# Performance work log

Hardware: AMD Instinct MI355X
Metric: run time of the kernel (lower is better)

Reference implementation:

```python
import jax, jax.numpy as jnp
import numpy as np

# Constants from init_kwargs
DT = 0.01
NIV = 8          # energy_input_dim[1]
HID = 64         # hidden_dims[0]
FEAT = 501       # per-field microstructure feature length (501+501=1002)


def _lin(k, fin, fout):
    return jax.random.normal(k, (fin, fout), dtype=jnp.float32) / np.sqrt(fin)


def setup_inputs() -> dict:
    key = jax.random.key(0)
    ks = jax.random.split(key, 12)
    B, T = 8192, 512
    e = jax.random.normal(ks[0], (B, T, 1), dtype=jnp.float32) * 0.1
    e_dot = jax.random.normal(ks[1], (B, T, 1), dtype=jnp.float32) * 0.1
    # positive microstructure fields (code computes nu**-1 and E/nu**2)
    E = jax.random.uniform(ks[2], (B, FEAT), minval=0.5, maxval=2.0, dtype=jnp.float32)
    nu = jax.random.uniform(ks[3], (B, FEAT), minval=0.5, maxval=2.0, dtype=jnp.float32)
    return {
        "e": e, "e_dot": e_dot, "E": E, "nu": nu,
        # EnergyFunction.B : Linear(1002,64) -> ReLU -> Linear(64,niv)
        "Bw1": _lin(ks[4], 2 * FEAT, HID), "Bb1": jnp.zeros((HID,), jnp.float32),
        "Bw2": _lin(ks[5], HID, NIV), "Bb2": jnp.zeros((NIV,), jnp.float32),
        # InverseDissipationPotential.beta : Linear(1002,64)->Softplus->Linear(64,niv)->Softplus
        "bw1": _lin(ks[6], 2 * FEAT, HID), "bb1": jnp.zeros((HID,), jnp.float32),
        "bw2": _lin(ks[7], HID, NIV), "bb2": jnp.zeros((NIV,), jnp.float32),
    }


def reference(e, e_dot, E, nu, Bw1, Bb1, Bw2, Bb2, bw1, bb1, bw2, bb2):
    # --- microstructure encoder (TrueFeatures) ---
    nu_p = 1.0 / jnp.mean(1.0 / nu, axis=1, keepdims=True)                 # [B,1]
    E_p = jnp.mean(E / nu ** 2, axis=1, keepdims=True) * nu_p ** 2         # [B,1]
    m = jnp.concatenate([E, nu], axis=-1)                                  # [B,1002]

    # Time-invariant MLP coefficients (hoisted out of the time loop)
    Bm = jax.nn.relu(m @ Bw1 + Bb1) @ Bw2 + Bb2                            # [B,NIV]
    beta = jax.nn.softplus(jax.nn.softplus(m @ bw1 + bb1) @ bw2 + bb2)     # [B,NIV]
    Bsum = jnp.sum(Bm, axis=-1, keepdims=True)                             # [B,1]

    B_, niv = Bm.shape
    xi0 = jnp.zeros((B_, niv), dtype=e.dtype)

    def step(xi, inp):
        u, p = inp                                                          # [B,1],[B,1]
        # Analytic gradients of L = sum_{b,k} Bm_bk * (0.5*E' u^2 + 0.5*(u-xi_k)^2 + 0.5*sum_j xi_j^2)
        du = u - xi                                                         # [B,NIV]
        grad_u = Bsum * E_p * u + jnp.sum(Bm * du, axis=-1, keepdims=True)  # [B,1] (s_eq)
        grad_v = -Bm * du + Bsum * xi                                       # [B,NIV] (d)
        q = -grad_v
        # Analytic gradients of potential = -0.5*nu' p^2 + 0.5*sum(beta*q^2)
        grad_p = -nu_p * p                                                  # [B,1] (s_neq)
        grad_q = beta * q                                                   # [B,NIV] (kinetics)
        stress = grad_u - grad_p
        return xi + DT * grad_q, (stress, xi)

    xs = (jnp.swapaxes(e, 0, 1), jnp.swapaxes(e_dot, 0, 1))                 # [T,B,1]
    _, (stress_t, xi_t) = jax.lax.scan(step, xi0, xs)
    stress = jnp.swapaxes(stress_t, 0, 1)                                   # [B,T,1]
    xi = jnp.swapaxes(xi_t, 0, 1)                                           # [B,T,NIV]
    return stress, xi
```

## Files before the change

### kernel.cpp

```cpp
#include <hip/hip_runtime.h>
#include <hip/hip_bf16.h>

#define FEATN 501
#define KPAD 1024
#define MSTRIDE 1032
#define NB 8192
#define NT 512
#define DTC 0.01f

typedef __attribute__((ext_vector_type(8))) short short8;
typedef __attribute__((ext_vector_type(4))) float f32x4;

__device__ __forceinline__ float softplus_f(float x) {
    return fmaxf(x, 0.f) + log1pf(expf(-fabsf(x)));
}
__device__ __forceinline__ ushort f2bf(float x) {
    __hip_bfloat16 h = __float2bfloat16(x);
    return *reinterpret_cast<ushort*>(&h);
}
__device__ __forceinline__ void gl_lds16(const void* g, void* l) {
    __builtin_amdgcn_global_load_lds(
        (const __attribute__((address_space(1))) void*)g,
        (__attribute__((address_space(3))) void*)l, 16, 0, 0);
}
__device__ __forceinline__ float dpp_add(float x, const int ctrl) {
    int s = __builtin_bit_cast(int, x);
    int y;
    switch (ctrl) {
    case 0xB1:  y = __builtin_amdgcn_update_dpp(0, s, 0xB1, 0xf, 0xf, true); break;
    case 0x4E:  y = __builtin_amdgcn_update_dpp(0, s, 0x4E, 0xf, 0xf, true); break;
    default:    y = __builtin_amdgcn_update_dpp(0, s, 0x141, 0xf, 0xf, true); break;
    }
    return x + __builtin_bit_cast(float, y);
}

__global__ __launch_bounds__(256) void wtrans_kernel(
    const float* __restrict__ Bw1, const float* __restrict__ bw1,
    ushort* __restrict__ Wt) {
    const int h = blockIdx.x;
    const float* W = (h < 64) ? Bw1 : bw1;
    const int col = h & 63;
    #pragma unroll
    for (int it = 0; it < 4; ++it) {
        const int k = it * 256 + threadIdx.x;
        const int ksrc = (k < FEATN) ? k
                       : (k >= 512 && k < 512 + FEATN) ? k - 11 : -1;
        const float v = (ksrc >= 0) ? W[(size_t)ksrc * 64 + col] : 0.f;
        Wt[(size_t)(((k >> 5) * 128 + h) * 4 + ((k >> 3) & 3)) * 8 + (k & 7)] =
            f2bf(v);
    }
}

__global__ __launch_bounds__(1024, 8) void enc_kernel(
    const float* __restrict__ E, const float* __restrict__ nu,
    const ushort* __restrict__ Wt,
    const float* __restrict__ Bb1, const float* __restrict__ bb1,
    const float* __restrict__ Bw2, const float* __restrict__ Bb2,
    const float* __restrict__ bw2, const float* __restrict__ bb2,
    float* __restrict__ cw) {
    __shared__ ushort Ml[16 * MSTRIDE];
    __shared__ float red[3][2048];
    __shared__ float hid[128][17];
    __shared__ float nups[16], Eps[16];

    const int tid = threadIdx.x;
    const int w = tid >> 6, lane = tid & 63;
    const int bb0 = blockIdx.x * 16;

    {
        const size_t base = (size_t)(bb0 + w) * FEATN;
        float s1 = 0.f, s2 = 0.f;
        for (int i = lane; i < FEATN; i += 64) {
            const float Ev = E[base + i];
            const float nv = nu[base + i];
            const float inv = 1.0f / nv;
            s1 += inv;
            s2 = fmaf(Ev, inv * inv, s2);
            Ml[w * MSTRIDE + i] = f2bf(Ev);
            Ml[w * MSTRIDE + 512 + i] = f2bf(nv);
        }
        if (lane < 11) {
            Ml[w * MSTRIDE + FEATN + lane] = 0;
            Ml[w * MSTRIDE + 512 + FEATN + lane] = 0;
        }
        #pragma unroll
        for (int o = 32; o; o >>= 1) {
            s1 += __shfl_xor(s1, o);
            s2 += __shfl_xor(s2, o);
        }
        if (lane == 0) {
            const float np = (float)FEATN / s1;
            nups[w] = np;
            Eps[w] = (s2 / (float)FEATN) * np * np;
        }
    }
    __syncthreads();

    const int g = w & 3, q = w >> 2;
    const int r15 = lane & 15, kg = lane >> 4;
    {
        const ushort* wbase = Wt + (size_t)(q * 8) * 4096;
        const int aoff = (g * 32 + r15) * 32 + kg * 8;
        const int boff = r15 * MSTRIDE + q * 256 + kg * 8;
        const int rot = blockIdx.x & 7;

        f32x4 acc0 = {0.f, 0.f, 0.f, 0.f}, acc1 = acc0;
        #pragma unroll
        for (int s = 0; s < 8; ++s) {
            const int ss = (s + rot) & 7;
            const short8 a0 = *(const short8*)(wbase + ss * 4096 + aoff);
            const short8 a1 = *(const short8*)(wbase + ss * 4096 + aoff + 512);
            const short8 b = *(const short8*)&Ml[boff + ss * 32];
            acc0 = __builtin_amdgcn_mfma_f32_16x16x32_bf16(a0, b, acc0, 0, 0, 0);
            acc1 = __builtin_amdgcn_mfma_f32_16x16x32_bf16(a1, b, acc1, 0, 0, 0);
        }
        if (q > 0) {
            *(f32x4*)&red[q - 1][(g * 64 + lane) * 8] = acc0;
            *(f32x4*)&red[q - 1][(g * 64 + lane) * 8 + 4] = acc1;
        }
        __syncthreads();
        if (q == 0) {
            #pragma unroll
            for (int p = 0; p < 3; ++p) {
                acc0 += *(const f32x4*)&red[p][(g * 64 + lane) * 8];
                acc1 += *(const f32x4*)&red[p][(g * 64 + lane) * 8 + 4];
            }
            #pragma unroll
            for (int t = 0; t < 2; ++t) {
                #pragma unroll
                for (int r = 0; r < 4; ++r) {
                    const int h = g * 32 + t * 16 + kg * 4 + r;
                    const float bias = (h < 64) ? Bb1[h] : bb1[h - 64];
                    float v = (t ? acc1[r] : acc0[r]) + bias;
                    v = (h < 64) ? fmaxf(v, 0.f) : softplus_f(v);
                    hid[h][r15] = v;
                }
            }
        }
    }
    __syncthreads();

    if (tid < 128) {
        const int bl = tid >> 3, k = tid & 7;
        float dB = 0.f, db = 0.f;
        #pragma unroll 8
        for (int h = 0; h < 64; ++h) {
            dB = fmaf(hid[h][bl], Bw2[h * 8 + k], dB);
            db = fmaf(hid[64 + h][bl], bw2[h * 8 + k], db);
        }
        const float Bm = dB + Bb2[k];
        const float be = softplus_f(db + bb2[k]);
        float Bs = Bm;
        Bs += __shfl_xor(Bs, 1);
        Bs += __shfl_xor(Bs, 2);
        Bs += __shfl_xor(Bs, 4);
        float* cb = cw + (size_t)(bb0 + bl) * 32;
        cb[k] = 1.f - DTC * be * (Bm + Bs);
        cb[8 + k] = DTC * be * Bm;
        cb[16 + k] = Bm;
        if (k == 0) {
            cb[24] = Bs * (Eps[bl] + 1.f);
            cb[25] = nups[bl];
        }
    }
}

__global__ __launch_bounds__(256) void time_kernel(
    const float* __restrict__ e, const float* __restrict__ ed,
    const float* __restrict__ cw, float* __restrict__ stress,
    float* __restrict__ xi_out) {
    __shared__ float els[4][512];
    __shared__ float pls[4][512];
    const int wv = threadIdx.x >> 6;
    const int wid = (blockIdx.x << 2) + wv;
    const int lane = threadIdx.x & 63;
    const int j = lane >> 3, k = lane & 7;

    const float* eb = e + (size_t)wid * NT;
    const float* edb = ed + (size_t)wid * NT;
    gl_lds16(eb + lane * 4, &els[wv][0]);
    gl_lds16(eb + 256 + lane * 4, &els[wv][256]);
    gl_lds16(edb + lane * 4, &pls[wv][0]);
    gl_lds16(edb + 256 + lane * 4, &pls[wv][256]);

    const float* cb = cw + (size_t)wid * 32;
    const float a = cb[k];
    const float c = cb[8 + k];
    const float Bm = cb[16 + k];
    const float sE2 = cb[24];
    const float nup = cb[25];
    asm volatile("s_waitcnt vmcnt(0)" ::: "memory");

    const float a2 = a * a, a4 = a2 * a2;
    float A = 1.f;
    if (j & 1) A *= a;
    if (j & 2) A *= a2;
    if (j & 4) A *= a4;
    float pw[8];
    {
        float run = c;
        #pragma unroll
        for (int i = 7; i >= 0; --i) {
            const bool on = (i < j);
            pw[i] = on ? run : 0.f;
            run = on ? run * a : run;
        }
    }

    float* xb = xi_out + (size_t)wid * (NT * 8);
    float* sb = stress + (size_t)wid * NT;
    const float* el = &els[wv][0];
    const float* pl = &pls[wv][0];

    float xs = 0.f;
    #pragma unroll
    for (int it = 0; it < 64; ++it) {
        const int t0 = it * 8;
        const float4 q0 = *(const float4*)(el + t0);
        const float4 q1 = *(const float4*)(el + t0 + 4);
        const float cuj = el[t0 + j];
        const float cpj = pl[t0 + j];
        float xi_j = A * xs;
        xi_j = fmaf(pw[0], q0.x, xi_j);
        xi_j = fmaf(pw[1], q0.y, xi_j);
        xi_j = fmaf(pw[2], q0.z, xi_j);
        xi_j = fmaf(pw[3], q0.w, xi_j);
        xi_j = fmaf(pw[4], q1.x, xi_j);
        xi_j = fmaf(pw[5], q1.y, xi_j);
        xi_j = fmaf(pw[6], q1.z, xi_j);
        xi_j = fmaf(pw[7], q1.w, xi_j);
        xb[t0 * 8 + lane] = xi_j;
        float r = Bm * xi_j;
        r = dpp_add(r, 0xB1);
        r = dpp_add(r, 0x4E);
        r = dpp_add(r, 0x141);
        if (k == 0)
            sb[t0 + j] = fmaf(cuj, sE2, fmaf(nup, cpj, -r));
        xs = fmaf(a, __shfl(xi_j, 56 + k), c * q1.w);
    }
}

extern "C" void kernel_launch(void* const* d_in, const int* in_sizes, int n_in,
                              void* d_out, int out_size, void* d_ws, size_t ws_size,
                              hipStream_t stream) {
    const float* e   = (const float*)d_in[0];
    const float* ed  = (const float*)d_in[1];
    const float* E   = (const float*)d_in[2];
    const float* nu  = (const float*)d_in[3];
    const float* Bw1 = (const float*)d_in[4];
    const float* Bb1 = (const float*)d_in[5];
    const float* Bw2 = (const float*)d_in[6];
    const float* Bb2 = (const float*)d_in[7];
    const float* bw1 = (const float*)d_in[8];
    const float* bb1 = (const float*)d_in[9];
    const float* bw2 = (const float*)d_in[10];
    const float* bb2 = (const float*)d_in[11];

    float* out = (float*)d_out;
    float* stress = out;
    float* xi = out + (size_t)NB * NT;
    ushort* Wt = (ushort*)d_ws;
    float* cw = (float*)((char*)d_ws + (1 << 20));

    wtrans_kernel<<<128, 256, 0, stream>>>(Bw1, bw1, Wt);
    enc_kernel<<<512, 1024, 0, stream>>>(E, nu, Wt, Bb1, bb1,
                                         Bw2, Bb2, bw2, bb2, cw);
    time_kernel<<<2048, 256, 0, stream>>>(e, ed, cw, stress, xi);
}
```

Measured before the change: 59.43 us.

## Split encoder prep into separate kernel staging bf16 features in output scratch

Moves the per-row reductions and the bf16 conversion of E/nu out of the encoder into a separate 2048-block prep kernel. That kernel writes the packed features into the unused xi output buffer and the nu_p/E_p scalars into the coefficient workspace. The encoder then loads its tile with direct global-to-LDS copies and a lower occupancy hint. The aim is to spread the memory-bound prep over more blocks, at the cost of an extra launch and a global round trip. It relies on time_kernel later overwriting xi.

```diff
diff --git a/kernel.cpp b/kernel.cpp
--- a/kernel.cpp
+++ b/kernel.cpp
@@ -51,8 +51,42 @@
     }
 }
 
-__global__ __launch_bounds__(1024, 8) void enc_kernel(
+__global__ __launch_bounds__(256) void prep_kernel(
     const float* __restrict__ E, const float* __restrict__ nu,
+    float* __restrict__ xi, float* __restrict__ cw) {
+    const int b = blockIdx.x * 4 + (threadIdx.x >> 6);
+    const int lane = threadIdx.x & 63;
+    const size_t base = (size_t)b * FEATN;
+    ushort* mb = (ushort*)(xi + (size_t)b * 4096 + 512);
+    float s1 = 0.f, s2 = 0.f;
+    for (int i = lane; i < FEATN; i += 64) {
+        const float Ev = E[base + i];
+        const float nv = nu[base + i];
+        const float inv = 1.0f / nv;
+        s1 += inv;
+        s2 = fmaf(Ev, inv * inv, s2);
+        mb[i] = f2bf(Ev);
+        mb[512 + i] = f2bf(nv);
+    }
+    if (lane < 11) {
+        mb[FEATN + lane] = 0;
+        mb[512 + FEATN + lane] = 0;
+    }
+    #pragma unroll
+    for (int o = 32; o; o >>= 1) {
+        s1 += __shfl_xor(s1, o);
+        s2 += __shfl_xor(s2, o);
+    }
+    if (lane == 0) {
+        const float np = (float)FEATN / s1;
+        float* cb = cw + (size_t)b * 32;
+        cb[26] = np;
+        cb[27] = (s2 / (float)FEATN) * np * np;
+    }
+}
+
+__global__ __launch_bounds__(1024, 4) void encb_kernel(
+    const float* __restrict__ xi,
     const ushort* __restrict__ Wt,
     const float* __restrict__ Bb1, const float* __restrict__ bb1,
     const float* __restrict__ Bw2, const float* __restrict__ Bb2,
@@ -61,43 +95,21 @@
     __shared__ ushort Ml[16 * MSTRIDE];
     __shared__ float red[3][2048];
     __shared__ float hid[128][17];
-    __shared__ float nups[16], Eps[16];
 
     const int tid = threadIdx.x;
     const int w = tid >> 6, lane = tid & 63;
     const int bb0 = blockIdx.x * 16;
-
-    {
-        const size_t base = (size_t)(bb0 + w) * FEATN;
-        float s1 = 0.f, s2 = 0.f;
-        for (int i = lane; i < FEATN; i += 64) {
-            const float Ev = E[base + i];
-            const float nv = nu[base + i];
-            const float inv = 1.0f / nv;
-            s1 += inv;
-            s2 = fmaf(Ev, inv * inv, s2);
-            Ml[w * MSTRIDE + i] = f2bf(Ev);
-            Ml[w * MSTRIDE + 512 + i] = f2bf(nv);
-        }
-        if (lane < 11) {
-            Ml[w * MSTRIDE + FEATN + lane] = 0;
-            Ml[w * MSTRIDE + 512 + FEATN + lane] = 0;
-        }
-        #pragma unroll
-        for (int o = 32; o; o >>= 1) {
-            s1 += __shfl_xor(s1, o);
-            s2 += __shfl_xor(s2, o);
-        }
-        if (lane == 0) {
-            const float np = (float)FEATN / s1;
-            nups[w] = np;
-            Eps[w] = (s2 / (float)FEATN) * np * np;
-        }
-    }
-    __syncthreads();
-
     const int g = w & 3, q = w >> 2;
     const int r15 = lane & 15, kg = lane >> 4;
+
+    {
+        const ushort* mb = (const ushort*)(xi + (size_t)(bb0 + w) * 4096 + 512);
+        gl_lds16(mb + lane * 8, &Ml[w * MSTRIDE]);
+        gl_lds16(mb + 512 + lane * 8, &Ml[w * MSTRIDE + 512]);
+    }
+    asm volatile("s_waitcnt vmcnt(0)" ::: "memory");
+    __syncthreads();
+
     {
         const ushort* wbase = Wt + (size_t)(q * 8) * 4096;
         const int aoff = (g * 32 + r15) * 32 + kg * 8;
@@ -159,8 +171,8 @@
         cb[8 + k] = DTC * be * Bm;
         cb[16 + k] = Bm;
         if (k == 0) {
-            cb[24] = Bs * (Eps[bl] + 1.f);
-            cb[25] = nups[bl];
+            cb[24] = Bs * (cb[27] + 1.f);
+            cb[25] = cb[26];
         }
     }
 }
@@ -263,7 +275,8 @@
     float* cw = (float*)((char*)d_ws + (1 << 20));
 
     wtrans_kernel<<<128, 256, 0, stream>>>(Bw1, bw1, Wt);
-    enc_kernel<<<512, 1024, 0, stream>>>(E, nu, Wt, Bb1, bb1,
-                                         Bw2, Bb2, bw2, bb2, cw);
+    prep_kernel<<<2048, 256, 0, stream>>>(E, nu, xi, cw);
+    encb_kernel<<<512, 1024, 0, stream>>>(xi, Wt, Bb1, bb1,
+                                          Bw2, Bb2, bw2, bb2, cw);
     time_kernel<<<2048, 256, 0, stream>>>(e, ed, cw, stress, xi);
 }
```

Measured after the change: 69.14 us. +16.3%, slower.
